# Kernel tuning notes

Measured on AMD Instinct MI355X. Metric: run time of the kernel, lower is better.

The kernel has to match this reference:

```python
import jax, jax.numpy as jnp
import numpy as np
from jax import lax

B, T, S = 8, 512, 512
E, H, V = 512, 1024, 32000
K, L, ML = 3, 6, 1024
PAD_IDX = 1  # padding value used to fill conv left-padding (module quirk: fills with trg_pad_idx)


def setup_inputs() -> dict:
    key = jax.random.key(0)
    ks = jax.random.split(key, 20)
    s = 0.02
    return {
        "trg": jax.random.randint(ks[0], (B, T), 0, V),
        "encoder_conved": jax.random.normal(ks[1], (B, S, E), jnp.float32),
        "encoder_combined": jax.random.normal(ks[2], (B, S, E), jnp.float32),
        "tok_emb": jax.random.normal(ks[3], (V, E), jnp.float32) * s,
        "pos_emb": jax.random.normal(ks[4], (ML, E), jnp.float32) * s,
        "emb2hid_w": jax.random.normal(ks[5], (E, H), jnp.float32) * s,
        "emb2hid_b": jnp.zeros((H,), jnp.float32),
        "hid2emb_w": jax.random.normal(ks[6], (H, E), jnp.float32) * s,
        "hid2emb_b": jnp.zeros((E,), jnp.float32),
        "attn_hid2emb_w": jax.random.normal(ks[7], (H, E), jnp.float32) * s,
        "attn_hid2emb_b": jnp.zeros((E,), jnp.float32),
        "attn_emb2hid_w": jax.random.normal(ks[8], (E, H), jnp.float32) * s,
        "attn_emb2hid_b": jnp.zeros((H,), jnp.float32),
        "fc_out_w": jax.random.normal(ks[9], (E, V), jnp.float32) * s,
        "fc_out_b": jnp.zeros((V,), jnp.float32),
        "conv_w": jax.random.normal(ks[10], (L, 2 * H, H, K), jnp.float32) * s,
        "conv_b": jnp.zeros((L, 2 * H), jnp.float32),
    }


def reference(trg, encoder_conved, encoder_combined, tok_emb, pos_emb,
              emb2hid_w, emb2hid_b, hid2emb_w, hid2emb_b,
              attn_hid2emb_w, attn_hid2emb_b, attn_emb2hid_w, attn_emb2hid_b,
              fc_out_w, fc_out_b, conv_w, conv_b):
    scale = jnp.sqrt(jnp.float32(0.5))
    # embeddings: (B, T, E)
    embedded = tok_emb[trg] + pos_emb[jnp.arange(T)][None, :, :]
    # emb -> hid, move to channels-first: (B, H, T)
    conv_input = jnp.transpose(embedded @ emb2hid_w + emb2hid_b, (0, 2, 1))

    pad = jnp.full((B, H, K - 1), jnp.float32(PAD_IDX))
    dn = lax.conv_dimension_numbers((B, H, T + K - 1), (2 * H, H, K), ('NCH', 'OIH', 'NCH'))

    for l in range(L):
        padded = jnp.concatenate([pad, conv_input], axis=2)  # (B, H, T+K-1)
        conved = lax.conv_general_dilated(padded, conv_w[l], (1,), 'VALID',
                                          dimension_numbers=dn)
        conved = conved + conv_b[l][None, :, None]  # (B, 2H, T)
        a, g = jnp.split(conved, 2, axis=1)
        conved = a * jax.nn.sigmoid(g)  # GLU -> (B, H, T)
        # attention
        conved_emb = jnp.transpose(conved, (0, 2, 1)) @ attn_hid2emb_w + attn_hid2emb_b  # (B,T,E)
        combined = (conved_emb + embedded) * scale
        energy = jnp.einsum('bte,bse->bts', combined, encoder_conved)
        attention = jax.nn.softmax(energy, axis=2)
        attended = jnp.einsum('bts,bse->bte', attention, encoder_combined)
        attended = attended @ attn_emb2hid_w + attn_emb2hid_b  # (B,T,H)
        conved = (conved + jnp.transpose(attended, (0, 2, 1))) * scale
        conv_input = (conved + conv_input) * scale

    conv_output = jnp.transpose(conv_input, (0, 2, 1)) @ hid2emb_w + hid2emb_b  # (B,T,E)
    pred_output = conv_output @ fc_out_w + fc_out_b  # (B,T,V)
    return pred_output
```

## Files before the change

### kernel.cpp

```cpp
#include <hip/hip_runtime.h>

typedef __bf16 bf16_t;
typedef __bf16 bf16x8 __attribute__((ext_vector_type(8)));
typedef float f32x4 __attribute__((ext_vector_type(4)));

#define SQH 0.70710678118654752440f

__device__ __forceinline__ void gld_lds16(const bf16_t* g, bf16_t* l) {
  __builtin_amdgcn_global_load_lds(
      (__attribute__((address_space(1))) void*)(void*)(g),
      (__attribute__((address_space(3))) void*)(l), 16, 0, 0);
}

__global__ __launch_bounds__(256, 2)
void k_gemm_nt(const bf16_t* __restrict__ A, const bf16_t* __restrict__ B,
               const float* __restrict__ bias,
               float* __restrict__ Cf, bf16_t* __restrict__ Cb,
               int K, int lda, int ldb, int ldc, int ldcb,
               int pad2, int bshift, int seglog2, int clog2,
               int cbpad2, int cbshift,
               long long saB, long long sbB, long long scB)
{
  __shared__ __align__(16) bf16_t sA[128 * 32];
  __shared__ __align__(16) bf16_t sB[128 * 32];

  const int tid  = threadIdx.x;
  const int wave = tid >> 6;
  const int lane = tid & 63;
  const int z    = blockIdx.z;
  A += (long long)z * saB;
  B += (long long)z * sbB;
  if (Cf) Cf += (long long)z * scB;
  if (Cb) Cb += (long long)z * scB;

  const int m0 = blockIdx.y * 128;
  const int n0 = blockIdx.x * 128;

  const int rq = tid >> 2;
  const int qo = (tid & 3) * 8;

  bf16_t* lA0 = sA + wave * 512;
  bf16_t* lA1 = sA + 2048 + wave * 512;
  bf16_t* lB0 = sB + wave * 512;
  bf16_t* lB1 = sB + 2048 + wave * 512;

  const int wm = (wave & 1) * 64;
  const int wn = (wave >> 1) * 64;
  const int lm = lane & 15;
  const int lk = (lane >> 4) * 8;

  f32x4 acc[4][4] = {};
  const int kmask = (1 << seglog2) - 1;

  for (int k0 = 0; k0 < K; k0 += 32) {
    const int kseg = k0 >> seglog2;
    const int kcol = k0 & kmask;
    {
      const int m1 = m0 + rq;
      const int m2 = m1 + 64;
      const long long ar1 = m1 + pad2 * (m1 >> clog2) + bshift + kseg;
      const long long ar2 = m2 + pad2 * (m2 >> clog2) + bshift + kseg;
      gld_lds16(A + ar1 * lda + kcol + qo, lA0);
      gld_lds16(A + ar2 * lda + kcol + qo, lA1);
      const long long nr = n0 + rq;
      gld_lds16(B + nr * ldb + k0 + qo, lB0);
      gld_lds16(B + (nr + 64) * ldb + k0 + qo, lB1);
    }
    __syncthreads();
    bf16x8 af[4], bfr[4];
#pragma unroll
    for (int i = 0; i < 4; ++i)
      af[i] = *(const bf16x8*)(sA + (wm + i * 16 + lm) * 32 + lk);
#pragma unroll
    for (int j = 0; j < 4; ++j)
      bfr[j] = *(const bf16x8*)(sB + (wn + j * 16 + lm) * 32 + lk);
#pragma unroll
    for (int i = 0; i < 4; ++i)
#pragma unroll
      for (int j = 0; j < 4; ++j)
        acc[i][j] = __builtin_amdgcn_mfma_f32_16x16x32_bf16(af[i], bfr[j], acc[i][j], 0, 0, 0);
    __syncthreads();
  }

  const int lq = (lane >> 4) * 4;
#pragma unroll
  for (int i = 0; i < 4; ++i) {
#pragma unroll
    for (int j = 0; j < 4; ++j) {
      const int col = n0 + wn + j * 16 + lm;
      const float bv = bias ? bias[col] : 0.0f;
#pragma unroll
      for (int r = 0; r < 4; ++r) {
        const int row = m0 + wm + i * 16 + lq + r;
        const float v = acc[i][j][r] + bv;
        if (Cf) Cf[(long long)row * ldc + col] = v;
        if (Cb) {
          const long long brow = row + cbpad2 * (row >> clog2) + cbshift;
          Cb[brow * ldcb + col] = (bf16_t)v;
        }
      }
    }
  }
}

__global__ void k_transpose(const float* __restrict__ in, bf16_t* __restrict__ out,
                            int R, int C, long long sIn, long long sOut) {
  __shared__ float tile[32][33];
  const int b = blockIdx.z;
  in  += (long long)b * sIn;
  out += (long long)b * sOut;
  const int c0 = blockIdx.x * 32;
  const int r0 = blockIdx.y * 32;
  const int tx = threadIdx.x;
  for (int i = threadIdx.y; i < 32; i += 8) {
    int r = r0 + i, c = c0 + tx;
    tile[i][tx] = (r < R && c < C) ? in[(long long)r * C + c] : 0.f;
  }
  __syncthreads();
  for (int i = threadIdx.y; i < 32; i += 8) {
    int c = c0 + i, r = r0 + tx;
    if (c < C && r < R) out[(long long)c * R + r] = (bf16_t)tile[tx][i];
  }
}

__global__ void k_convert(const float* __restrict__ in, bf16_t* __restrict__ out, int n) {
  int i = blockIdx.x * 256 + threadIdx.x;
  if (i < n) out[i] = (bf16_t)in[i];
}

__global__ void k_convw(const float* __restrict__ in, bf16_t* __restrict__ out) {
  const long long s = blockIdx.y;
  const int i = blockIdx.x * 256 + threadIdx.x;
  const float* p = in + s * 3072 + (long long)i * 3;
  float w0 = p[0], w1 = p[1], w2 = p[2];
  bf16_t* q = out + s * 3072;
  q[i] = (bf16_t)w0; q[1024 + i] = (bf16_t)w1; q[2048 + i] = (bf16_t)w2;
}

__global__ void k_embed(const int* __restrict__ trg, const float* __restrict__ tok,
                        const float* __restrict__ pos,
                        float* __restrict__ embF, bf16_t* __restrict__ embB) {
  const long long bt = blockIdx.x;
  const int t = (int)(bt & 511);
  const int id = trg[bt];
  const float* tp = tok + (long long)id * 512;
  const float* pp = pos + (long long)t * 512;
  for (int j = threadIdx.x; j < 512; j += 256) {
    float v = tp[j] + pp[j];
    embF[bt * 512 + j] = v;
    embB[bt * 512 + j] = (bf16_t)v;
  }
}

__global__ void k_padinit(bf16_t* __restrict__ Xp) {
  const int i = blockIdx.x * 256 + threadIdx.x;
  const int b = i >> 11;
  const int r = (i >> 10) & 1;
  const int h = i & 1023;
  Xp[((long long)b * 514 + r) * 1024 + h] = (bf16_t)1.0f;
}

__global__ void k_glu(const float* __restrict__ C, float* __restrict__ oF,
                      bf16_t* __restrict__ oB) {
  const long long m = blockIdx.x;
  const float* row = C + m * 2048;
  for (int h = threadIdx.x; h < 1024; h += 256) {
    float a = row[h], g = row[1024 + h];
    float v = a * (1.f / (1.f + __expf(-g)));
    oF[m * 1024 + h] = v;
    oB[m * 1024 + h] = (bf16_t)v;
  }
}

__global__ void k_combine(const float* __restrict__ a, const float* __restrict__ b,
                          bf16_t* __restrict__ o, int n) {
  int i = blockIdx.x * 256 + threadIdx.x;
  if (i < n) o[i] = (bf16_t)((a[i] + b[i]) * SQH);
}

__global__ void k_softmax(const float* __restrict__ E, bf16_t* __restrict__ A) {
  __shared__ float red[8];
  const long long m = blockIdx.x;
  const float* row = E + m * 512;
  const int t = threadIdx.x;
  float x0 = row[t], x1 = row[t + 256];
  float mx = fmaxf(x0, x1);
#pragma unroll
  for (int o = 32; o >= 1; o >>= 1) mx = fmaxf(mx, __shfl_xor(mx, o));
  const int w = t >> 6;
  if ((t & 63) == 0) red[w] = mx;
  __syncthreads();
  mx = fmaxf(fmaxf(red[0], red[1]), fmaxf(red[2], red[3]));
  float e0 = __expf(x0 - mx), e1 = __expf(x1 - mx);
  float s = e0 + e1;
#pragma unroll
  for (int o = 32; o >= 1; o >>= 1) s += __shfl_xor(s, o);
  if ((t & 63) == 0) red[4 + w] = s;
  __syncthreads();
  s = red[4] + red[5] + red[6] + red[7];
  float inv = 1.f / s;
  A[m * 512 + t]       = (bf16_t)(e0 * inv);
  A[m * 512 + t + 256] = (bf16_t)(e1 * inv);
}

__global__ void k_resid(const float* __restrict__ conved, const float* __restrict__ att2,
                        float* __restrict__ X, bf16_t* __restrict__ Xp) {
  const long long i = (long long)blockIdx.x * 256 + threadIdx.x;
  float v = ((conved[i] + att2[i]) * SQH + X[i]) * SQH;
  X[i] = v;
  const long long m = i >> 10;
  const int h = (int)(i & 1023);
  Xp[(m + 2 * (m >> 9) + 2) * 1024 + h] = (bf16_t)v;
}

extern "C" void kernel_launch(void* const* d_in, const int* in_sizes, int n_in,
                              void* d_out, int out_size, void* d_ws, size_t ws_size,
                              hipStream_t stream) {
  (void)in_sizes; (void)n_in; (void)out_size; (void)ws_size;
  const int*   trg    = (const int*)  d_in[0];
  const float* encCv  = (const float*)d_in[1];
  const float* encCb  = (const float*)d_in[2];
  const float* tokE   = (const float*)d_in[3];
  const float* posE   = (const float*)d_in[4];
  const float* e2h_w  = (const float*)d_in[5];
  const float* e2h_b  = (const float*)d_in[6];
  const float* h2e_w  = (const float*)d_in[7];
  const float* h2e_b  = (const float*)d_in[8];
  const float* ah2e_w = (const float*)d_in[9];
  const float* ah2e_b = (const float*)d_in[10];
  const float* ae2h_w = (const float*)d_in[11];
  const float* ae2h_b = (const float*)d_in[12];
  const float* fc_w   = (const float*)d_in[13];
  const float* fc_b   = (const float*)d_in[14];
  const float* convW  = (const float*)d_in[15];
  const float* convB  = (const float*)d_in[16];
  float* out = (float*)d_out;

  char* cur = (char*)d_ws;
  auto alloc = [&](long long bytes) { char* r = cur; cur += (bytes + 255) & ~255LL; return (void*)r; };

  bf16_t* embA    = (bf16_t*)alloc(4096LL * 512 * 2);
  bf16_t* Xpad    = (bf16_t*)alloc(8LL * 514 * 1024 * 2);
  bf16_t* convedB = (bf16_t*)alloc(4096LL * 1024 * 2);
  bf16_t* combB   = (bf16_t*)alloc(4096LL * 512 * 2);
  bf16_t* attnB   = (bf16_t*)alloc(4096LL * 512 * 2);
  bf16_t* attdB   = (bf16_t*)alloc(4096LL * 512 * 2);
  bf16_t* coutB   = (bf16_t*)alloc(4096LL * 512 * 2);
  bf16_t* wT_e2h  = (bf16_t*)alloc(1024LL * 512 * 2);
  bf16_t* wT_ah2e = (bf16_t*)alloc(512LL * 1024 * 2);
  bf16_t* wT_ae2h = (bf16_t*)alloc(1024LL * 512 * 2);
  bf16_t* wT_h2e  = (bf16_t*)alloc(512LL * 1024 * 2);
  bf16_t* wT_fc   = (bf16_t*)alloc(32000LL * 512 * 2);
  bf16_t* encCvB  = (bf16_t*)alloc(8LL * 512 * 512 * 2);
  bf16_t* encTcb  = (bf16_t*)alloc(8LL * 512 * 512 * 2);
  bf16_t* convWT  = (bf16_t*)alloc(6LL * 2048 * 3072 * 2);
  float*  embF    = (float*)alloc(4096LL * 512 * 4);
  float*  Xf      = (float*)alloc(4096LL * 1024 * 4);
  float*  convC   = (float*)alloc(4096LL * 2048 * 4);
  float*  convedF = (float*)alloc(4096LL * 1024 * 4);
  float*  tmpE    = (float*)alloc(4096LL * 512 * 4);
  float*  energy  = (float*)alloc(4096LL * 512 * 4);
  float*  att2    = (float*)alloc(4096LL * 1024 * 4);

  const dim3 tb(32, 8);
  k_transpose<<<dim3(32, 16, 1),  tb, 0, stream>>>(e2h_w,  wT_e2h,  512, 1024, 0, 0);
  k_transpose<<<dim3(16, 32, 1),  tb, 0, stream>>>(ah2e_w, wT_ah2e, 1024, 512, 0, 0);
  k_transpose<<<dim3(32, 16, 1),  tb, 0, stream>>>(ae2h_w, wT_ae2h, 512, 1024, 0, 0);
  k_transpose<<<dim3(16, 32, 1),  tb, 0, stream>>>(h2e_w,  wT_h2e,  1024, 512, 0, 0);
  k_transpose<<<dim3(1000, 16, 1),tb, 0, stream>>>(fc_w,   wT_fc,   512, 32000, 0, 0);
  k_transpose<<<dim3(16, 16, 8),  tb, 0, stream>>>(encCb,  encTcb,  512, 512, 512LL * 512, 512LL * 512);
  k_convert<<<8192, 256, 0, stream>>>(encCv, encCvB, 8 * 512 * 512);
  k_convw<<<dim3(4, 12288), 256, 0, stream>>>(convW, convWT);
  k_embed<<<4096, 256, 0, stream>>>(trg, tokE, posE, embF, embA);
  k_padinit<<<64, 256, 0, stream>>>(Xpad);

  auto gemm = [&](const bf16_t* A, const bf16_t* B, const float* bias,
                  float* Cf, bf16_t* Cb, int M, int N, int K,
                  int lda, int ldb, int ldc, int ldcb,
                  int pad2, int bshift, int seglog2,
                  int cbpad2, int cbshift,
                  long long saB, long long sbB, long long scB, int Z) {
    dim3 g(N / 128, M / 128, Z);
    k_gemm_nt<<<g, 256, 0, stream>>>(A, B, bias, Cf, Cb, K, lda, ldb, ldc, ldcb,
                                     pad2, bshift, seglog2, 9, cbpad2, cbshift,
                                     saB, sbB, scB);
  };

  gemm(embA, wT_e2h, e2h_b, Xf, Xpad, 4096, 1024, 512,
       512, 512, 1024, 1024, 0, 0, 30, 2, 2, 0, 0, 0, 1);

  for (int l = 0; l < 6; ++l) {
    gemm(Xpad, convWT + (long long)l * 2048 * 3072, convB + l * 2048, convC, nullptr,
         4096, 2048, 3072, 1024, 3072, 2048, 0, 2, 0, 10, 0, 0, 0, 0, 0, 1);
    k_glu<<<4096, 256, 0, stream>>>(convC, convedF, convedB);
    gemm(convedB, wT_ah2e, ah2e_b, tmpE, nullptr, 4096, 512, 1024,
         1024, 1024, 512, 0, 0, 0, 30, 0, 0, 0, 0, 0, 1);
    k_combine<<<8192, 256, 0, stream>>>(tmpE, embF, combB, 4096 * 512);
    gemm(combB, encCvB, nullptr, energy, nullptr, 512, 512, 512,
         512, 512, 512, 0, 0, 0, 30, 0, 0, 512LL * 512, 512LL * 512, 512LL * 512, 8);
    k_softmax<<<4096, 256, 0, stream>>>(energy, attnB);
    gemm(attnB, encTcb, nullptr, nullptr, attdB, 512, 512, 512,
         512, 512, 512, 512, 0, 0, 30, 0, 0, 512LL * 512, 512LL * 512, 512LL * 512, 8);
    gemm(attdB, wT_ae2h, ae2h_b, att2, nullptr, 4096, 1024, 512,
         512, 512, 1024, 0, 0, 0, 30, 0, 0, 0, 0, 0, 1);
    k_resid<<<16384, 256, 0, stream>>>(convedF, att2, Xf, Xpad);
  }

  gemm(Xpad, wT_h2e, h2e_b, nullptr, coutB, 4096, 512, 1024,
       1024, 1024, 512, 512, 2, 2, 30, 0, 0, 0, 0, 0, 1);
  gemm(coutB, wT_fc, fc_b, out, nullptr, 4096, 32000, 512,
       512, 512, 32000, 0, 0, 0, 30, 0, 0, 0, 0, 0, 1);
}
```

Measured before the change: 2.165 ms.

## Fuse GLU, combine and residual epilogues into GEMM kernels via template modes

Templates the GEMM kernel on an epilogue mode and fuses the GLU, the combine-with-embedding step and the residual update into the epilogues of the conv, attn_hid2emb and attn_emb2hid GEMMs. Conv weight and bias output channels are interleaved so each value/gate pair lands in adjacent lanes and can be joined with a lane shuffle. This drops three elementwise kernels per layer and the fp32 intermediate buffers they read and wrote (convC, tmpE, att2). The cost is that half the lanes sit idle in the GLU store and the stores become stride-2 scattered writes.

```diff
diff --git a/kernel.cpp b/kernel.cpp
--- a/kernel.cpp
+++ b/kernel.cpp
@@ -12,10 +12,12 @@
       (__attribute__((address_space(3))) void*)(l), 16, 0, 0);
 }
 
+template<int MODE>
 __global__ __launch_bounds__(256, 2)
 void k_gemm_nt(const bf16_t* __restrict__ A, const bf16_t* __restrict__ B,
                const float* __restrict__ bias,
                float* __restrict__ Cf, bf16_t* __restrict__ Cb,
+               const float* __restrict__ aux0, float* __restrict__ aux1,
                int K, int lda, int ldb, int ldc, int ldcb,
                int pad2, int bshift, int seglog2, int clog2,
                int cbpad2, int cbshift,
@@ -92,11 +94,30 @@
 #pragma unroll
       for (int r = 0; r < 4; ++r) {
         const int row = m0 + wm + i * 16 + lq + r;
-        const float v = acc[i][j][r] + bv;
-        if (Cf) Cf[(long long)row * ldc + col] = v;
-        if (Cb) {
+        float v = acc[i][j][r] + bv;
+        if constexpr (MODE == 0) {
+          if (Cf) Cf[(long long)row * ldc + col] = v;
+          if (Cb) {
+            const long long brow = row + cbpad2 * (row >> clog2) + cbshift;
+            Cb[brow * ldcb + col] = (bf16_t)v;
+          }
+        } else if constexpr (MODE == 1) {
+          float p = __shfl_xor(v, 1);
+          if (!(lane & 1)) {
+            float res = v * (1.f / (1.f + __expf(-p)));
+            const int h = col >> 1;
+            Cf[(long long)row * 1024 + h] = res;
+            Cb[(long long)row * 1024 + h] = (bf16_t)res;
+          }
+        } else if constexpr (MODE == 2) {
+          float c = (v + aux0[(long long)row * ldc + col]) * SQH;
+          Cb[(long long)row * ldcb + col] = (bf16_t)c;
+        } else {
+          const long long idx = (long long)row * ldc + col;
+          float nv = ((aux0[idx] + v) * SQH + aux1[idx]) * SQH;
+          aux1[idx] = nv;
           const long long brow = row + cbpad2 * (row >> clog2) + cbshift;
-          Cb[brow * ldcb + col] = (bf16_t)v;
+          Cb[brow * ldcb + col] = (bf16_t)nv;
         }
       }
     }
@@ -133,8 +154,19 @@
   const int i = blockIdx.x * 256 + threadIdx.x;
   const float* p = in + s * 3072 + (long long)i * 3;
   float w0 = p[0], w1 = p[1], w2 = p[2];
-  bf16_t* q = out + s * 3072;
+  const int l = (int)(s >> 11);
+  const int o = (int)(s & 2047);
+  const int onew = (o < 1024) ? (o << 1) : (((o - 1024) << 1) | 1);
+  bf16_t* q = out + ((long long)(l << 11) + onew) * 3072;
   q[i] = (bf16_t)w0; q[1024 + i] = (bf16_t)w1; q[2048 + i] = (bf16_t)w2;
+}
+
+__global__ void k_convb(const float* __restrict__ in, float* __restrict__ out) {
+  const int i = blockIdx.x * 256 + threadIdx.x;
+  const int l = i >> 11;
+  const int o = i & 2047;
+  const int onew = (o < 1024) ? (o << 1) : (((o - 1024) << 1) | 1);
+  out[(l << 11) + onew] = in[i];
 }
 
 __global__ void k_embed(const int* __restrict__ trg, const float* __restrict__ tok,
@@ -160,24 +192,6 @@
   Xp[((long long)b * 514 + r) * 1024 + h] = (bf16_t)1.0f;
 }
 
-__global__ void k_glu(const float* __restrict__ C, float* __restrict__ oF,
-                      bf16_t* __restrict__ oB) {
-  const long long m = blockIdx.x;
-  const float* row = C + m * 2048;
-  for (int h = threadIdx.x; h < 1024; h += 256) {
-    float a = row[h], g = row[1024 + h];
-    float v = a * (1.f / (1.f + __expf(-g)));
-    oF[m * 1024 + h] = v;
-    oB[m * 1024 + h] = (bf16_t)v;
-  }
-}
-
-__global__ void k_combine(const float* __restrict__ a, const float* __restrict__ b,
-                          bf16_t* __restrict__ o, int n) {
-  int i = blockIdx.x * 256 + threadIdx.x;
-  if (i < n) o[i] = (bf16_t)((a[i] + b[i]) * SQH);
-}
-
 __global__ void k_softmax(const float* __restrict__ E, bf16_t* __restrict__ A) {
   __shared__ float red[8];
   const long long m = blockIdx.x;
@@ -201,16 +215,6 @@
   float inv = 1.f / s;
   A[m * 512 + t]       = (bf16_t)(e0 * inv);
   A[m * 512 + t + 256] = (bf16_t)(e1 * inv);
-}
-
-__global__ void k_resid(const float* __restrict__ conved, const float* __restrict__ att2,
-                        float* __restrict__ X, bf16_t* __restrict__ Xp) {
-  const long long i = (long long)blockIdx.x * 256 + threadIdx.x;
-  float v = ((conved[i] + att2[i]) * SQH + X[i]) * SQH;
-  X[i] = v;
-  const long long m = i >> 10;
-  const int h = (int)(i & 1023);
-  Xp[(m + 2 * (m >> 9) + 2) * 1024 + h] = (bf16_t)v;
 }
 
 extern "C" void kernel_launch(void* const* d_in, const int* in_sizes, int n_in,
@@ -254,13 +258,11 @@
   bf16_t* encCvB  = (bf16_t*)alloc(8LL * 512 * 512 * 2);
   bf16_t* encTcb  = (bf16_t*)alloc(8LL * 512 * 512 * 2);
   bf16_t* convWT  = (bf16_t*)alloc(6LL * 2048 * 3072 * 2);
+  float*  biasI   = (float*)alloc(6LL * 2048 * 4);
   float*  embF    = (float*)alloc(4096LL * 512 * 4);
   float*  Xf      = (float*)alloc(4096LL * 1024 * 4);
-  float*  convC   = (float*)alloc(4096LL * 2048 * 4);
   float*  convedF = (float*)alloc(4096LL * 1024 * 4);
-  float*  tmpE    = (float*)alloc(4096LL * 512 * 4);
   float*  energy  = (float*)alloc(4096LL * 512 * 4);
-  float*  att2    = (float*)alloc(4096LL * 1024 * 4);
 
   const dim3 tb(32, 8);
   k_transpose<<<dim3(32, 16, 1),  tb, 0, stream>>>(e2h_w,  wT_e2h,  512, 1024, 0, 0);
@@ -271,43 +273,46 @@
   k_transpose<<<dim3(16, 16, 8),  tb, 0, stream>>>(encCb,  encTcb,  512, 512, 512LL * 512, 512LL * 512);
   k_convert<<<8192, 256, 0, stream>>>(encCv, encCvB, 8 * 512 * 512);
   k_convw<<<dim3(4, 12288), 256, 0, stream>>>(convW, convWT);
+  k_convb<<<48, 256, 0, stream>>>(convB, biasI);
   k_embed<<<4096, 256, 0, stream>>>(trg, tokE, posE, embF, embA);
   k_padinit<<<64, 256, 0, stream>>>(Xpad);
 
-  auto gemm = [&](const bf16_t* A, const bf16_t* B, const float* bias,
-                  float* Cf, bf16_t* Cb, int M, int N, int K,
-                  int lda, int ldb, int ldc, int ldcb,
-                  int pad2, int bshift, int seglog2,
-                  int cbpad2, int cbshift,
-                  long long saB, long long sbB, long long scB, int Z) {
+  auto gemm0 = [&](const bf16_t* A, const bf16_t* B, const float* bias,
+                   float* Cf, bf16_t* Cb, int M, int N, int K,
+                   int lda, int ldb, int ldc, int ldcb,
+                   int pad2, int bshift, int seglog2,
+                   int cbpad2, int cbshift,
+                   long long saB, long long sbB, long long scB, int Z) {
     dim3 g(N / 128, M / 128, Z);
-    k_gemm_nt<<<g, 256, 0, stream>>>(A, B, bias, Cf, Cb, K, lda, ldb, ldc, ldcb,
-                                     pad2, bshift, seglog2, 9, cbpad2, cbshift,
-                                     saB, sbB, scB);
+    k_gemm_nt<0><<<g, 256, 0, stream>>>(A, B, bias, Cf, Cb, nullptr, nullptr,
+                                        K, lda, ldb, ldc, ldcb,
+                                        pad2, bshift, seglog2, 9, cbpad2, cbshift,
+                                        saB, sbB, scB);
   };
 
-  gemm(embA, wT_e2h, e2h_b, Xf, Xpad, 4096, 1024, 512,
-       512, 512, 1024, 1024, 0, 0, 30, 2, 2, 0, 0, 0, 1);
+  gemm0(embA, wT_e2h, e2h_b, Xf, Xpad, 4096, 1024, 512,
+        512, 512, 1024, 1024, 0, 0, 30, 2, 2, 0, 0, 0, 1);
 
   for (int l = 0; l < 6; ++l) {
-    gemm(Xpad, convWT + (long long)l * 2048 * 3072, convB + l * 2048, convC, nullptr,
-         4096, 2048, 3072, 1024, 3072, 2048, 0, 2, 0, 10, 0, 0, 0, 0, 0, 1);
-    k_glu<<<4096, 256, 0, stream>>>(convC, convedF, convedB);
-    gemm(convedB, wT_ah2e, ah2e_b, tmpE, nullptr, 4096, 512, 1024,
-         1024, 1024, 512, 0, 0, 0, 30, 0, 0, 0, 0, 0, 1);
-    k_combine<<<8192, 256, 0, stream>>>(tmpE, embF, combB, 4096 * 512);
-    gemm(combB, encCvB, nullptr, energy, nullptr, 512, 512, 512,
-         512, 512, 512, 0, 0, 0, 30, 0, 0, 512LL * 512, 512LL * 512, 512LL * 512, 8);
+    k_gemm_nt<1><<<dim3(16, 32, 1), 256, 0, stream>>>(
+        Xpad, convWT + (long long)l * 2048 * 3072, biasI + l * 2048,
+        convedF, convedB, nullptr, nullptr,
+        3072, 1024, 3072, 1024, 1024, 2, 0, 10, 9, 0, 0, 0, 0, 0);
+    k_gemm_nt<2><<<dim3(4, 32, 1), 256, 0, stream>>>(
+        convedB, wT_ah2e, ah2e_b, nullptr, combB, embF, nullptr,
+        1024, 1024, 1024, 512, 512, 0, 0, 30, 9, 0, 0, 0, 0, 0);
+    gemm0(combB, encCvB, nullptr, energy, nullptr, 512, 512, 512,
+          512, 512, 512, 0, 0, 0, 30, 0, 0, 512LL * 512, 512LL * 512, 512LL * 512, 8);
     k_softmax<<<4096, 256, 0, stream>>>(energy, attnB);
-    gemm(attnB, encTcb, nullptr, nullptr, attdB, 512, 512, 512,
-         512, 512, 512, 512, 0, 0, 30, 0, 0, 512LL * 512, 512LL * 512, 512LL * 512, 8);
-    gemm(attdB, wT_ae2h, ae2h_b, att2, nullptr, 4096, 1024, 512,
-         512, 512, 1024, 0, 0, 0, 30, 0, 0, 0, 0, 0, 1);
-    k_resid<<<16384, 256, 0, stream>>>(convedF, att2, Xf, Xpad);
-  }
-
-  gemm(Xpad, wT_h2e, h2e_b, nullptr, coutB, 4096, 512, 1024,
-       1024, 1024, 512, 512, 2, 2, 30, 0, 0, 0, 0, 0, 1);
-  gemm(coutB, wT_fc, fc_b, out, nullptr, 4096, 32000, 512,
-       512, 512, 32000, 0, 0, 0, 30, 0, 0, 0, 0, 0, 1);
-}
+    gemm0(attnB, encTcb, nullptr, nullptr, attdB, 512, 512, 512,
+          512, 512, 512, 512, 0, 0, 30, 0, 0, 512LL * 512, 512LL * 512, 512LL * 512, 8);
+    k_gemm_nt<3><<<dim3(8, 32, 1), 256, 0, stream>>>(
+        attdB, wT_ae2h, ae2h_b, nullptr, Xpad, convedF, Xf,
+        512, 512, 512, 1024, 1024, 0, 0, 30, 9, 2, 2, 0, 0, 0);
+  }
+
+  gemm0(Xpad, wT_h2e, h2e_b, nullptr, coutB, 4096, 512, 1024,
+        1024, 1024, 512, 512, 2, 2, 30, 0, 0, 0, 0, 0, 1);
+  gemm0(coutB, wT_fc, fc_b, out, nullptr, 4096, 32000, 512,
+        512, 512, 32000, 0, 0, 0, 30, 0, 0, 0, 0, 0, 1);
+}
```

New measurement: 2.052 ms. 5.2% less time.
